# Performance work log

Measured on AMD Instinct MI355X. Metric: run time of the kernel, lower is better.

Reference implementation:

```python
import jax, jax.numpy as jnp
import numpy as np

B, H, W, C = 32, 32, 32, 512
N_GROUPS = 32
EPS = 1e-5


def group_norm(x, scale, bias, n_groups=N_GROUPS, eps=EPS):
    b, h, w, c = x.shape
    xg = x.reshape(b, h, w, n_groups, c // n_groups)
    mean = xg.mean(axis=(1, 2, 4), keepdims=True)
    var = xg.var(axis=(1, 2, 4), keepdims=True)
    xg = (xg - mean) * jax.lax.rsqrt(var + eps)
    return xg.reshape(b, h, w, c) * scale + bias


def setup_inputs() -> dict:
    key = jax.random.key(0)
    ks = jax.random.split(key, 8)
    x = jax.random.normal(ks[0], (B, H, W, C), dtype=jnp.float32)
    t = jax.random.normal(ks[1], (B,), dtype=jnp.float32)
    gn_scale = jnp.ones((C,), jnp.float32)
    gn_bias = jnp.zeros((C,), jnp.float32)
    w_qkv = jax.random.normal(ks[2], (C, 3 * C), dtype=jnp.float32) / np.sqrt(C)
    b_qkv = jnp.zeros((3 * C,), jnp.float32)
    w_out = jax.random.normal(ks[3], (C, C), dtype=jnp.float32) / np.sqrt(C)
    b_out = jnp.zeros((C,), jnp.float32)
    return {"x": x, "t": t, "gn_scale": gn_scale, "gn_bias": gn_bias,
            "w_qkv": w_qkv, "b_qkv": b_qkv, "w_out": w_out, "b_out": b_out}


def reference(x, t, gn_scale, gn_bias, w_qkv, b_qkv, w_out, b_out):
    b, h, w, c = x.shape
    z = group_norm(x, gn_scale, gn_bias)
    qkv = jnp.einsum('bhwc,cd->bhwd', z, w_qkv) + b_qkv  # [b,h,w,3C]
    q, k, v = jnp.split(qkv, 3, axis=-1)
    # single-head spatial attention over all h*w positions
    attn = jnp.einsum('bhwc,bHWc->bhwHW', q, k) / jnp.sqrt(jnp.asarray(c, x.dtype))
    attn = jax.nn.softmax(attn.reshape(b, h, w, h * w), axis=-1)
    attn = attn.reshape(b, h, w, h, w)
    scores = jnp.einsum('bhwHW,bHWc->bhwc', attn, v)
    scores = jnp.einsum('bhwc,cd->bhwd', scores, w_out) + b_out
    return x + scores
```

## Files before the change

### kernel.cpp

```cpp
#include <hip/hip_runtime.h>

typedef unsigned short u16;
typedef short bf16x8 __attribute__((ext_vector_type(8)));
typedef float f32x4 __attribute__((ext_vector_type(4)));

__device__ __forceinline__ u16 f2bf(float f) {
  union { float f; unsigned u; } c; c.f = f;
  unsigned r = (c.u + 0x7FFFu + ((c.u >> 16) & 1u)) >> 16;
  return (u16)r;
}
__device__ __forceinline__ float bf2f(u16 h) {
  union { unsigned u; float f; } c; c.u = ((unsigned)h) << 16;
  return c.f;
}
__device__ __forceinline__ void gload16(const void* g, void* l) {
  __builtin_amdgcn_global_load_lds(
      (const __attribute__((address_space(1))) unsigned*)g,
      (__attribute__((address_space(3))) unsigned*)l, 16, 0, 0);
}

__global__ __launch_bounds__(256) void prep_weights(
    const float* __restrict__ w_qkv, const float* __restrict__ w_out,
    u16* __restrict__ wqkvT, u16* __restrict__ woutT) {
  int i = blockIdx.x * 256 + threadIdx.x;
  const int T1 = 1536 * 512;
  if (i < T1) {
    int n = i >> 9, c = i & 511;
    wqkvT[i] = f2bf(w_qkv[(size_t)c * 1536 + n]);
  } else {
    int j = i - T1;
    int n = j >> 9, c = j & 511;
    woutT[j] = f2bf(w_out[(size_t)c * 512 + n]);
  }
}

__global__ __launch_bounds__(256) void groupnorm_k(
    const float* __restrict__ x, const float* __restrict__ scale,
    const float* __restrict__ bias, u16* __restrict__ z) {
  const int blk = blockIdx.x, b = blk >> 5, g = blk & 31;
  const float* xb = x + (size_t)b * 524288 + g * 16;
  u16* zb = z + (size_t)b * 524288 + g * 16;
  const int tid = threadIdx.x, lane = tid & 63, wid = tid >> 6;

  float4 vv[16];
  float s = 0.f, ss = 0.f;
#pragma unroll
  for (int i = 0; i < 16; ++i) {
    int e = (i * 256 + tid) * 4;
    int hw = e >> 4, j = e & 15;
    vv[i] = *(const float4*)&xb[(size_t)hw * 512 + j];
    s += vv[i].x + vv[i].y + vv[i].z + vv[i].w;
    ss += vv[i].x * vv[i].x + vv[i].y * vv[i].y + vv[i].z * vv[i].z + vv[i].w * vv[i].w;
  }
#pragma unroll
  for (int off = 32; off; off >>= 1) {
    s += __shfl_xor(s, off);
    ss += __shfl_xor(ss, off);
  }
  __shared__ float rs[4], rq[4];
  if (!lane) { rs[wid] = s; rq[wid] = ss; }
  __syncthreads();
  float S_ = rs[0] + rs[1] + rs[2] + rs[3];
  float Q_ = rq[0] + rq[1] + rq[2] + rq[3];
  const float inv_n = 1.f / 16384.f;
  float mean = S_ * inv_n;
  float var = Q_ * inv_n - mean * mean;
  float rstd = rsqrtf(var + 1e-5f);

  int j0 = (tid * 4) & 15;
  float sc0 = scale[g * 16 + j0 + 0] * rstd, sc1 = scale[g * 16 + j0 + 1] * rstd;
  float sc2 = scale[g * 16 + j0 + 2] * rstd, sc3 = scale[g * 16 + j0 + 3] * rstd;
  float bi0 = bias[g * 16 + j0 + 0] - mean * sc0, bi1 = bias[g * 16 + j0 + 1] - mean * sc1;
  float bi2 = bias[g * 16 + j0 + 2] - mean * sc2, bi3 = bias[g * 16 + j0 + 3] - mean * sc3;
#pragma unroll
  for (int i = 0; i < 16; ++i) {
    int e = (i * 256 + tid) * 4;
    int hw = e >> 4, j = e & 15;
    ushort4 o;
    o.x = f2bf(vv[i].x * sc0 + bi0);
    o.y = f2bf(vv[i].y * sc1 + bi1);
    o.z = f2bf(vv[i].z * sc2 + bi2);
    o.w = f2bf(vv[i].w * sc3 + bi3);
    *(ushort4*)&zb[(size_t)hw * 512 + j] = o;
  }
}

#define QSCALE 0.04419417382415922f

template <int EPI>
__global__ __launch_bounds__(512, 2) void gemm_ring(
    const u16* __restrict__ A, const u16* __restrict__ Bt,
    int gx, int gxy, int N, int K,
    int sched, int sp1, int sp2,
    long long sAb, long long sBb, long long sCb,
    const float* __restrict__ bias, const float* __restrict__ resid,
    u16* __restrict__ qb, u16* __restrict__ kb, u16* __restrict__ vt,
    u16* __restrict__ outb, float* __restrict__ outf,
    float* __restrict__ lsum) {
  const int orig = blockIdx.x;
  const int xcd = orig & 7, jj = orig >> 3;
  int id;
  if (sched == 0) {
    int pan = jj % gx, loc = jj / gx;
    id = (xcd * sp1 + loc) * gx + pan;
  } else {
    int tile = jj % gxy, bl = jj / gxy;
    id = (xcd * sp2 + bl) * gxy + tile;
  }
  const int z = id / gxy;
  const int r2 = id - z * gxy;
  const int by = r2 / gx, bx = r2 - by * gx;

  const u16* Ab = A + (size_t)z * sAb;
  const u16* Bb = Bt + (size_t)z * sBb;

  __shared__ u16 As[4][8192];
  __shared__ u16 Bs[4][8192];

  const int tid = threadIdx.x;
  const int lane = tid & 63, wid = tid >> 6;
  const int wm = wid & 1, wn = wid >> 1;
  const int l15 = lane & 15, l4 = lane >> 4;
  const int m0 = by * 256, n0 = bx * 256;

  const int lrs = tid >> 3;
  const int g0 = (tid & 7) ^ (lrs & 7);
  const int ra = (lrs << 1) | (g0 >> 2);
  const int ko = (g0 & 3) << 3;

  const int lrb = l15 >> 1;
  const int gg = ((l15 & 1) << 2) | l4;
  const int gsw = gg ^ lrb;
  const int aoff = wm * 4096 + lrb * 64 + gsw * 8;
  const int boff = (wn >> 1) * 4096 + (wn & 1) * 2048 + lrb * 64 + gsw * 8;

  f32x4 acc[8][4];
#pragma unroll
  for (int i = 0; i < 8; ++i)
#pragma unroll
    for (int j = 0; j < 4; ++j)
#pragma unroll
      for (int r = 0; r < 4; ++r) acc[i][j][r] = 0.f;

  const int NT = K >> 5;

  auto stA = [&](int sb, int t2) {
    const u16* s0 = Ab + (size_t)(m0 + ra) * K + t2 * 32 + ko;
    const u16* s1 = Ab + (size_t)(m0 + 128 + ra) * K + t2 * 32 + ko;
    gload16(s0, &As[sb][tid * 8]);
    gload16(s1, &As[sb][4096 + tid * 8]);
  };
  auto stB = [&](int sb, int t2) {
    const u16* s0 = Bb + (size_t)(n0 + ra) * K + t2 * 32 + ko;
    const u16* s1 = Bb + (size_t)(n0 + 128 + ra) * K + t2 * 32 + ko;
    gload16(s0, &Bs[sb][tid * 8]);
    gload16(s1, &Bs[sb][4096 + tid * 8]);
  };

#define TILE_BODY(P, TT, DOSTG, WN)                                            \
  do {                                                                         \
    if (DOSTG) { stA(((P) + 3) & 3, (TT) + 3); stB(((P) + 3) & 3, (TT) + 3); } \
    bf16x8 bq[4], af0[4], af1[4];                                              \
    _Pragma("unroll") for (int ni = 0; ni < 4; ++ni)                           \
        bq[ni] = *(const bf16x8*)&Bs[P][boff + ni * 512];                      \
    _Pragma("unroll") for (int i = 0; i < 4; ++i)                              \
        af0[i] = *(const bf16x8*)&As[P][aoff + i * 512];                       \
    _Pragma("unroll") for (int i = 0; i < 4; ++i)                              \
        af1[i] = *(const bf16x8*)&As[P][aoff + 2048 + i * 512];                \
    __builtin_amdgcn_s_setprio(1);                                             \
    _Pragma("unroll") for (int i = 0; i < 4; ++i)                              \
        _Pragma("unroll") for (int ni = 0; ni < 4; ++ni)                       \
            acc[i][ni] = __builtin_amdgcn_mfma_f32_16x16x32_bf16(              \
                af0[i], bq[ni], acc[i][ni], 0, 0, 0);                          \
    _Pragma("unroll") for (int i = 0; i < 4; ++i)                              \
        _Pragma("unroll") for (int ni = 0; ni < 4; ++ni)                       \
            acc[4 + i][ni] = __builtin_amdgcn_mfma_f32_16x16x32_bf16(          \
                af1[i], bq[ni], acc[4 + i][ni], 0, 0, 0);                      \
    __builtin_amdgcn_s_setprio(0);                                             \
    if ((WN) == 8) asm volatile("s_waitcnt vmcnt(8)" ::: "memory");            \
    else if ((WN) == 4) asm volatile("s_waitcnt vmcnt(4)" ::: "memory");       \
    else if ((WN) == 0) asm volatile("s_waitcnt vmcnt(0)" ::: "memory");       \
    if ((WN) >= -1) __builtin_amdgcn_s_barrier();                              \
  } while (0)

  stA(0, 0); stB(0, 0);
  stA(1, 1); stB(1, 1);
  stA(2, 2); stB(2, 2);
  asm volatile("s_waitcnt vmcnt(8)" ::: "memory");
  __builtin_amdgcn_s_barrier();

  int t = 0;
  for (; t + 7 < NT; t += 4) {
    TILE_BODY(0, t, 1, 8);
    TILE_BODY(1, t + 1, 1, 8);
    TILE_BODY(2, t + 2, 1, 8);
    TILE_BODY(3, t + 3, 1, 8);
  }
  TILE_BODY(0, t, 1, 8);
  TILE_BODY(1, t + 1, 0, 4);
  TILE_BODY(2, t + 2, 0, 0);
  TILE_BODY(3, t + 3, 0, -2);

#undef TILE_BODY

  if (EPI == 0) {
#pragma unroll
    for (int mi = 0; mi < 8; ++mi) {
#pragma unroll
      for (int ni = 0; ni < 4; ++ni) {
        const int gr0 = m0 + wm * 128 + mi * 16 + l4 * 4;
        const int gc = n0 + wn * 64 + ni * 16 + l15;
        const int bsel = gc >> 9, cin = gc & 511;
        const float bs = bias[gc];
        if (bsel < 2) {
          u16* dst = bsel ? kb : qb;
#pragma unroll
          for (int r = 0; r < 4; ++r) {
            float vvv = acc[mi][ni][r] + bs;
            if (bsel == 0) vvv *= QSCALE;
            dst[(size_t)(gr0 + r) * 512 + cin] = f2bf(vvv);
          }
        } else {
          ushort4 o;
          o.x = f2bf(acc[mi][ni][0] + bs);
          o.y = f2bf(acc[mi][ni][1] + bs);
          o.z = f2bf(acc[mi][ni][2] + bs);
          o.w = f2bf(acc[mi][ni][3] + bs);
          const int bb = gr0 >> 10, p = gr0 & 1023;
          *(ushort4*)&vt[(size_t)bb * 524288 + (size_t)cin * 1024 + p] = o;
        }
      }
    }
  } else if (EPI == 2) {
#pragma unroll
    for (int mi = 0; mi < 8; ++mi) {
#pragma unroll
      for (int ni = 0; ni < 4; ++ni) {
        const int gr0 = m0 + wm * 128 + mi * 16 + l4 * 4;
        const int gc = n0 + wn * 64 + ni * 16 + l15;
#pragma unroll
        for (int r = 0; r < 4; ++r)
          outf[(size_t)(gr0 + r) * N + gc] =
              acc[mi][ni][r] + bias[gc] + resid[(size_t)(gr0 + r) * N + gc];
      }
    }
  } else if (EPI == 3) {
    float rs_[8][4];
#pragma unroll
    for (int mi = 0; mi < 8; ++mi)
#pragma unroll
      for (int r = 0; r < 4; ++r) rs_[mi][r] = 0.f;
#pragma unroll
    for (int mi = 0; mi < 8; ++mi) {
      const int gr0 = m0 + wm * 128 + mi * 16 + l4 * 4;
#pragma unroll
      for (int ni = 0; ni < 4; ++ni) {
        const int gc = n0 + wn * 64 + ni * 16 + l15;
#pragma unroll
        for (int r = 0; r < 4; ++r) {
          float e = __expf(acc[mi][ni][r]);
          rs_[mi][r] += e;
          outb[(size_t)z * sCb + (size_t)(gr0 + r) * N + gc] = f2bf(e);
        }
      }
    }
#pragma unroll
    for (int mi = 0; mi < 8; ++mi) {
      const int gr0 = m0 + wm * 128 + mi * 16 + l4 * 4;
#pragma unroll
      for (int r = 0; r < 4; ++r) {
        float v = rs_[mi][r];
        v += __shfl_xor(v, 1);
        v += __shfl_xor(v, 2);
        v += __shfl_xor(v, 4);
        v += __shfl_xor(v, 8);
        if (l15 == 0)
          lsum[((size_t)z * 1024 + gr0 + r) * 16 + bx * 4 + wn] = v;
      }
    }
  } else {
#pragma unroll
    for (int mi = 0; mi < 8; ++mi) {
      const int gr0 = m0 + wm * 128 + mi * 16 + l4 * 4;
      float inv[4];
#pragma unroll
      for (int r = 0; r < 4; ++r) {
        const float* lp = &lsum[((size_t)z * 1024 + gr0 + r) * 16];
        const float4 a0 = *(const float4*)&lp[0];
        const float4 a1 = *(const float4*)&lp[4];
        const float4 a2 = *(const float4*)&lp[8];
        const float4 a3 = *(const float4*)&lp[12];
        inv[r] = 1.0f / (a0.x + a0.y + a0.z + a0.w + a1.x + a1.y + a1.z + a1.w +
                         a2.x + a2.y + a2.z + a2.w + a3.x + a3.y + a3.z + a3.w);
      }
#pragma unroll
      for (int ni = 0; ni < 4; ++ni) {
        const int gc = n0 + wn * 64 + ni * 16 + l15;
#pragma unroll
        for (int r = 0; r < 4; ++r)
          outb[(size_t)z * sCb + (size_t)(gr0 + r) * N + gc] =
              f2bf(acc[mi][ni][r] * inv[r]);
      }
    }
  }
}

extern "C" void kernel_launch(void* const* d_in, const int* in_sizes, int n_in,
                              void* d_out, int out_size, void* d_ws, size_t ws_size,
                              hipStream_t stream) {
  const float* x = (const float*)d_in[0];
  const float* gn_scale = (const float*)d_in[2];
  const float* gn_bias = (const float*)d_in[3];
  const float* w_qkv = (const float*)d_in[4];
  const float* b_qkv = (const float*)d_in[5];
  const float* w_out = (const float*)d_in[6];
  const float* b_out = (const float*)d_in[7];
  float* out = (float*)d_out;

  char* ws = (char*)d_ws;
  const size_t MB = 1024ull * 1024ull;
  u16* qb = (u16*)(ws + 0 * MB);
  u16* kb = (u16*)(ws + 32 * MB);
  u16* vt = (u16*)(ws + 64 * MB);
  float* lsum = (float*)(ws + 96 * MB);
  u16* zO = (u16*)(ws + 128 * MB);
  u16* S = (u16*)(ws + 160 * MB);
  u16* wqkvT = (u16*)(ws + 224 * MB);
  u16* woutT = (u16*)(ws + 226 * MB);

  prep_weights<<<4096, 256, 0, stream>>>(w_qkv, w_out, wqkvT, woutT);
  groupnorm_k<<<1024, 256, 0, stream>>>(x, gn_scale, gn_bias, zO);

  gemm_ring<0><<<768, 512, 0, stream>>>(
      zO, wqkvT, 6, 768, 1536, 512, 0, 16, 0, 0, 0, 0, b_qkv, nullptr,
      qb, kb, vt, nullptr, nullptr, nullptr);

  gemm_ring<3><<<512, 512, 0, stream>>>(
      qb, kb, 4, 16, 1024, 512, 1, 0, 4, 1024 * 512, 1024 * 512, 1024 * 1024,
      nullptr, nullptr, nullptr, nullptr, nullptr, S, nullptr, lsum);

  gemm_ring<4><<<256, 512, 0, stream>>>(
      S, vt, 2, 8, 512, 1024, 1, 0, 4, 1024 * 1024, 512 * 1024, 1024 * 512,
      nullptr, nullptr, nullptr, nullptr, nullptr, zO, nullptr, lsum);

  gemm_ring<2><<<256, 512, 0, stream>>>(
      zO, woutT, 2, 256, 512, 512, 0, 16, 0, 0, 0, 0, b_out, x,
      nullptr, nullptr, nullptr, nullptr, out, nullptr);
}
```

Measured before the change: 271.0 us.

## Fuse QK^T, softmax and PV into a single flash-attention kernel

Replaces the separate score GEMM (with exp epilogue and partial row sums) and the normalised PV GEMM with one flash-style kernel. Each block keeps 128 queries in registers, streams K and V^T tiles of 32 keys through double-buffered LDS, and accumulates exp(scores)·V directly, normalising at the end. This removes writing and re-reading the bf16 score matrix and the lsum buffer. In exchange it needs a large register footprint (128 output accumulators plus Q fragments under a 2-blocks-per-CU bound), uses small KV tiles with a barrier every iteration, and launches only 256 blocks, so spills or low occupancy could offset the saved traffic.

```diff
diff --git a/kernel.cpp b/kernel.cpp
--- a/kernel.cpp
+++ b/kernel.cpp
@@ -95,8 +95,7 @@
     long long sAb, long long sBb, long long sCb,
     const float* __restrict__ bias, const float* __restrict__ resid,
     u16* __restrict__ qb, u16* __restrict__ kb, u16* __restrict__ vt,
-    u16* __restrict__ outb, float* __restrict__ outf,
-    float* __restrict__ lsum) {
+    u16* __restrict__ outb, float* __restrict__ outf) {
   const int orig = blockIdx.x;
   const int xcd = orig & 7, jj = orig >> 3;
   int id;
@@ -231,7 +230,7 @@
         }
       }
     }
-  } else if (EPI == 2) {
+  } else {
 #pragma unroll
     for (int mi = 0; mi < 8; ++mi) {
 #pragma unroll
@@ -244,65 +243,129 @@
               acc[mi][ni][r] + bias[gc] + resid[(size_t)(gr0 + r) * N + gc];
       }
     }
-  } else if (EPI == 3) {
-    float rs_[8][4];
-#pragma unroll
-    for (int mi = 0; mi < 8; ++mi)
-#pragma unroll
-      for (int r = 0; r < 4; ++r) rs_[mi][r] = 0.f;
-#pragma unroll
-    for (int mi = 0; mi < 8; ++mi) {
-      const int gr0 = m0 + wm * 128 + mi * 16 + l4 * 4;
-#pragma unroll
-      for (int ni = 0; ni < 4; ++ni) {
-        const int gc = n0 + wn * 64 + ni * 16 + l15;
-#pragma unroll
-        for (int r = 0; r < 4; ++r) {
-          float e = __expf(acc[mi][ni][r]);
-          rs_[mi][r] += e;
-          outb[(size_t)z * sCb + (size_t)(gr0 + r) * N + gc] = f2bf(e);
-        }
+  }
+}
+
+__global__ __launch_bounds__(512, 2) void flash_k(
+    const u16* __restrict__ qg, const u16* __restrict__ kg,
+    const u16* __restrict__ vtg, u16* __restrict__ Og) {
+  __shared__ u16 Ks[2][32 * 512];
+  __shared__ u16 Vs[2][512 * 40];
+  __shared__ u16 Ps[8][16 * 40];
+
+  const int tid = threadIdx.x, lane = tid & 63, wid = tid >> 6;
+  const int l15 = lane & 15, l4 = lane >> 4;
+  const int orig = blockIdx.x;
+  const int xcd = orig & 7, jj = orig >> 3;
+  const int z = xcd * 4 + (jj & 3);
+  const int qb0 = jj >> 2;
+
+  const u16* qz = qg + (size_t)(z * 1024 + qb0 * 128) * 512;
+  const u16* kz = kg + (size_t)z * 1024 * 512;
+  const u16* vz = vtg + (size_t)z * 512 * 1024;
+
+  const int krow_ = tid >> 6;
+  const int kgr = tid & 63;
+  const int kgs = (kgr & 56) | ((kgr & 7) ^ (krow_ & 7));
+  const int vrow_ = tid >> 2;
+  const int vkvg = (tid & 3) << 3;
+
+  auto stageK = [&](int t, int buf) {
+    const u16* src = kz + ((size_t)t * 32 + krow_) * 512 + kgs * 8;
+#pragma unroll
+    for (int s = 0; s < 4; ++s)
+      gload16(src + (size_t)s * 8 * 512, &Ks[buf][s * 4096 + tid * 8]);
+  };
+
+  bf16x8 vstg[4];
+  auto loadV = [&](int t) {
+#pragma unroll
+    for (int s = 0; s < 4; ++s)
+      vstg[s] = *(const bf16x8*)&vz[(size_t)(s * 128 + vrow_) * 1024 + t * 32 + vkvg];
+  };
+  auto writeV = [&](int buf) {
+#pragma unroll
+    for (int s = 0; s < 4; ++s)
+      *(bf16x8*)&Vs[buf][(s * 128 + vrow_) * 40 + vkvg] = vstg[s];
+  };
+
+  bf16x8 qf[16];
+#pragma unroll
+  for (int kf = 0; kf < 16; ++kf)
+    qf[kf] = *(const bf16x8*)&qz[(size_t)(wid * 16 + l15) * 512 + kf * 32 + l4 * 8];
+
+  f32x4 oacc[32];
+#pragma unroll
+  for (int i = 0; i < 32; ++i)
+#pragma unroll
+    for (int r = 0; r < 4; ++r) oacc[i][r] = 0.f;
+  float rsum[4] = {0.f, 0.f, 0.f, 0.f};
+
+  stageK(0, 0);
+  loadV(0);
+  writeV(0);
+  __syncthreads();
+
+  for (int t = 0; t < 32; ++t) {
+    const int cur = t & 1;
+    const bool pre = (t + 1 < 32);
+    if (pre) { stageK(t + 1, cur ^ 1); loadV(t + 1); }
+
+    f32x4 sacc[2];
+#pragma unroll
+    for (int nf = 0; nf < 2; ++nf)
+#pragma unroll
+      for (int r = 0; r < 4; ++r) sacc[nf][r] = 0.f;
+#pragma unroll
+    for (int kf = 0; kf < 16; ++kf) {
+#pragma unroll
+      for (int nf = 0; nf < 2; ++nf) {
+        const int kvr = nf * 16 + l15;
+        const int g = kf * 4 + l4;
+        const int gs = (g & 56) | ((g & 7) ^ (kvr & 7));
+        const bf16x8 bfr = *(const bf16x8*)&Ks[cur][kvr * 512 + gs * 8];
+        sacc[nf] = __builtin_amdgcn_mfma_f32_16x16x32_bf16(qf[kf], bfr, sacc[nf], 0, 0, 0);
       }
     }
-#pragma unroll
-    for (int mi = 0; mi < 8; ++mi) {
-      const int gr0 = m0 + wm * 128 + mi * 16 + l4 * 4;
+
+#pragma unroll
+    for (int nf = 0; nf < 2; ++nf)
 #pragma unroll
       for (int r = 0; r < 4; ++r) {
-        float v = rs_[mi][r];
-        v += __shfl_xor(v, 1);
-        v += __shfl_xor(v, 2);
-        v += __shfl_xor(v, 4);
-        v += __shfl_xor(v, 8);
-        if (l15 == 0)
-          lsum[((size_t)z * 1024 + gr0 + r) * 16 + bx * 4 + wn] = v;
+        const float e = __expf(sacc[nf][r]);
+        rsum[r] += e;
+        Ps[wid][(l4 * 4 + r) * 40 + nf * 16 + l15] = f2bf(e);
       }
+
+    if (pre) writeV(cur ^ 1);
+
+    const bf16x8 pa = *(const bf16x8*)&Ps[wid][l15 * 40 + l4 * 8];
+    __builtin_amdgcn_s_setprio(1);
+#pragma unroll
+    for (int nf = 0; nf < 32; ++nf) {
+      const bf16x8 vb = *(const bf16x8*)&Vs[cur][(nf * 16 + l15) * 40 + l4 * 8];
+      oacc[nf] = __builtin_amdgcn_mfma_f32_16x16x32_bf16(pa, vb, oacc[nf], 0, 0, 0);
     }
-  } else {
-#pragma unroll
-    for (int mi = 0; mi < 8; ++mi) {
-      const int gr0 = m0 + wm * 128 + mi * 16 + l4 * 4;
-      float inv[4];
-#pragma unroll
-      for (int r = 0; r < 4; ++r) {
-        const float* lp = &lsum[((size_t)z * 1024 + gr0 + r) * 16];
-        const float4 a0 = *(const float4*)&lp[0];
-        const float4 a1 = *(const float4*)&lp[4];
-        const float4 a2 = *(const float4*)&lp[8];
-        const float4 a3 = *(const float4*)&lp[12];
-        inv[r] = 1.0f / (a0.x + a0.y + a0.z + a0.w + a1.x + a1.y + a1.z + a1.w +
-                         a2.x + a2.y + a2.z + a2.w + a3.x + a3.y + a3.z + a3.w);
-      }
-#pragma unroll
-      for (int ni = 0; ni < 4; ++ni) {
-        const int gc = n0 + wn * 64 + ni * 16 + l15;
-#pragma unroll
-        for (int r = 0; r < 4; ++r)
-          outb[(size_t)z * sCb + (size_t)(gr0 + r) * N + gc] =
-              f2bf(acc[mi][ni][r] * inv[r]);
-      }
-    }
-  }
+    __builtin_amdgcn_s_setprio(0);
+    __syncthreads();
+  }
+
+#pragma unroll
+  for (int r = 0; r < 4; ++r) {
+    float v = rsum[r];
+    v += __shfl_xor(v, 1);
+    v += __shfl_xor(v, 2);
+    v += __shfl_xor(v, 4);
+    v += __shfl_xor(v, 8);
+    rsum[r] = 1.0f / v;
+  }
+  u16* orow = Og + (size_t)(z * 1024 + qb0 * 128 + wid * 16) * 512;
+#pragma unroll
+  for (int nf = 0; nf < 32; ++nf)
+#pragma unroll
+    for (int r = 0; r < 4; ++r)
+      orow[(size_t)(l4 * 4 + r) * 512 + nf * 16 + l15] =
+          f2bf(oacc[nf][r] * rsum[r]);
 }
 
 extern "C" void kernel_launch(void* const* d_in, const int* in_sizes, int n_in,
@@ -322,9 +385,7 @@
   u16* qb = (u16*)(ws + 0 * MB);
   u16* kb = (u16*)(ws + 32 * MB);
   u16* vt = (u16*)(ws + 64 * MB);
-  float* lsum = (float*)(ws + 96 * MB);
   u16* zO = (u16*)(ws + 128 * MB);
-  u16* S = (u16*)(ws + 160 * MB);
   u16* wqkvT = (u16*)(ws + 224 * MB);
   u16* woutT = (u16*)(ws + 226 * MB);
 
@@ -333,17 +394,11 @@
 
   gemm_ring<0><<<768, 512, 0, stream>>>(
       zO, wqkvT, 6, 768, 1536, 512, 0, 16, 0, 0, 0, 0, b_qkv, nullptr,
-      qb, kb, vt, nullptr, nullptr, nullptr);
-
-  gemm_ring<3><<<512, 512, 0, stream>>>(
-      qb, kb, 4, 16, 1024, 512, 1, 0, 4, 1024 * 512, 1024 * 512, 1024 * 1024,
-      nullptr, nullptr, nullptr, nullptr, nullptr, S, nullptr, lsum);
-
-  gemm_ring<4><<<256, 512, 0, stream>>>(
-      S, vt, 2, 8, 512, 1024, 1, 0, 4, 1024 * 1024, 512 * 1024, 1024 * 512,
-      nullptr, nullptr, nullptr, nullptr, nullptr, zO, nullptr, lsum);
+      qb, kb, vt, nullptr, nullptr);
+
+  flash_k<<<256, 512, 0, stream>>>(qb, kb, vt, zO);
 
   gemm_ring<2><<<256, 512, 0, stream>>>(
       zO, woutT, 2, 256, 512, 512, 0, 16, 0, 0, 0, 0, b_out, x,
-      nullptr, nullptr, nullptr, nullptr, out, nullptr);
-}
+      nullptr, nullptr, nullptr, nullptr, out);
+}
```

Result: faster. 257.9 us (-4.8%).
